# Performance work log

Hardware: AMD Instinct MI355X
Metric: run time of the kernel (lower is better)

Reference implementation:

```python
import jax, jax.numpy as jnp
import numpy as np

DIM = 1024
INTER = 1024
N_EXPERTS = 16
TOPK = 4
SHARED_INTER = 2 * INTER  # n_shared_experts * moe_inter_dim
T = 8192


def setup_inputs() -> dict:
    key = jax.random.key(0)
    ks = jax.random.split(key, 15)
    s = 0.02
    inp = {
        "x": jax.random.normal(ks[0], (T, DIM), jnp.float32),
        "gate_w": jax.random.normal(ks[1], (N_EXPERTS, DIM), jnp.float32) * s,
        # routed experts, stacked over expert axis
        "ew1": jax.random.normal(ks[2], (N_EXPERTS, INTER, DIM), jnp.float32) * s,
        "eb1": jax.random.normal(ks[3], (N_EXPERTS, INTER), jnp.float32) * s,
        "ew2": jax.random.normal(ks[4], (N_EXPERTS, DIM, INTER), jnp.float32) * s,
        "eb2": jax.random.normal(ks[5], (N_EXPERTS, DIM), jnp.float32) * s,
        "ew3": jax.random.normal(ks[6], (N_EXPERTS, INTER, DIM), jnp.float32) * s,
        "eb3": jax.random.normal(ks[7], (N_EXPERTS, INTER), jnp.float32) * s,
        # shared expert MLP (inter = 2 * moe_inter_dim)
        "sw1": jax.random.normal(ks[8], (SHARED_INTER, DIM), jnp.float32) * s,
        "sb1": jax.random.normal(ks[9], (SHARED_INTER,), jnp.float32) * s,
        "sw2": jax.random.normal(ks[10], (DIM, SHARED_INTER), jnp.float32) * s,
        "sb2": jax.random.normal(ks[11], (DIM,), jnp.float32) * s,
        "sw3": jax.random.normal(ks[12], (SHARED_INTER, DIM), jnp.float32) * s,
        "sb3": jax.random.normal(ks[13], (SHARED_INTER,), jnp.float32) * s,
    }
    return inp


def _ffn(x, w1, b1, w2, b2, w3, b3):
    # w2(silu(w1(x)) * w3(x))
    return (jax.nn.silu(x @ w1.T + b1) * (x @ w3.T + b3)) @ w2.T + b2


def reference(x, gate_w, ew1, eb1, ew2, eb2, ew3, eb3, sw1, sb1, sw2, sb2, sw3, sb3):
    # Gate: softmax scores in fp32 (n_groups=1 -> no group masking), top-k routing
    scores = jax.nn.softmax((x @ gate_w.T).astype(jnp.float32), axis=-1)  # [T, E]
    top_vals, idx = jax.lax.top_k(scores, TOPK)  # [T, K]
    weights = top_vals.astype(x.dtype)  # route_scale = 1.0, softmax score_func

    # Per-expert combine weight: zero for unselected experts.
    nT = x.shape[0]
    cw = jnp.zeros((nT, N_EXPERTS), x.dtype).at[
        jnp.arange(nT)[:, None], idx
    ].add(weights)  # [T, E]

    # Routed experts: masked-dense dispatch (weight 0 kills unselected terms)
    y = jnp.zeros_like(x)
    for e in range(N_EXPERTS):
        y = y + cw[:, e:e + 1] * _ffn(x, ew1[e], eb1[e], ew2[e], eb2[e], ew3[e], eb3[e])

    # Shared experts (always applied)
    z = _ffn(x, sw1, sb1, sw2, sb2, sw3, sb3)
    return y + z
```

## Files before the change

### kernel.cpp

```cpp
#include <hip/hip_runtime.h>
#include <cstdint>
#include <cstddef>

#define TOK     8192
#define DIMD    1024
#define INTERD  1024
#define NEXP    16
#define SINTER  2048
#define CAP256  36864
#define MAXT    144
#define HBLK    32

typedef __bf16 bf16_t;
typedef __bf16 bf16x8_t __attribute__((ext_vector_type(8)));
typedef __bf16 bf16x4_t __attribute__((ext_vector_type(4)));
typedef float  f32x4_t  __attribute__((ext_vector_type(4)));

__device__ __forceinline__ void gload_lds16(const bf16_t* g, bf16_t* l) {
  __builtin_amdgcn_global_load_lds((const __attribute__((address_space(1))) void*)g,
                                   (__attribute__((address_space(3))) void*)l,
                                   16, 0, 0);
}

__global__ void init_kernel(int* toklist, float* wtlist, int* tile_e, int* tile_rs) {
  int i = blockIdx.x * blockDim.x + threadIdx.x;
  if (i < CAP256) { toklist[i] = -1; wtlist[i] = 0.0f; }
  if (i < 512)    { tile_e[i] = -1; tile_rs[i] = 0; }
}

__global__ void cvt_kernel(const float* __restrict__ in, bf16_t* __restrict__ out, int n4) {
  int stride = gridDim.x * blockDim.x;
  for (int i = blockIdx.x * blockDim.x + threadIdx.x; i < n4; i += stride) {
    float4 v = ((const float4*)in)[i];
    bf16x4_t o;
    o[0] = (bf16_t)v.x; o[1] = (bf16_t)v.y; o[2] = (bf16_t)v.z; o[3] = (bf16_t)v.w;
    ((bf16x4_t*)out)[i] = o;
  }
}

__global__ void cvt_ileave(const float* __restrict__ s1, const float* __restrict__ s3,
                           bf16_t* __restrict__ dst, int total4, int esh) {
  int stride = gridDim.x * blockDim.x;
  int fmask = (1 << esh) - 1;
  for (int i = blockIdx.x * blockDim.x + threadIdx.x; i < total4; i += stride) {
    int k4 = i & 255;
    int fr = i >> 8;
    int e  = fr >> esh;
    int f  = fr & fmask;
    int p  = f >> 4, s = f & 15;
    int real = ((p >> 1) << 4) + s;
    size_t srow = ((size_t)e << (esh - 1)) + real;
    const float* src = ((p & 1) ? s3 : s1) + (srow << 10) + (k4 << 2);
    float4 v = *(const float4*)src;
    bf16x4_t o;
    o[0] = (bf16_t)v.x; o[1] = (bf16_t)v.y; o[2] = (bf16_t)v.z; o[3] = (bf16_t)v.w;
    ((bf16x4_t*)dst)[i] = o;
  }
}

__global__ __launch_bounds__(256)
void gate_kernel(const float* __restrict__ x, const float* __restrict__ gw,
                 int* __restrict__ tkidx, float* __restrict__ tkwt) {
  int wv = threadIdx.x >> 6, lane = threadIdx.x & 63;
  int t = blockIdx.x * 4 + wv;
  const float4* xp = (const float4*)(x + (size_t)t * DIMD + lane * 16);
  float4 xv[4];
#pragma unroll
  for (int i = 0; i < 4; ++i) xv[i] = xp[i];
  float sc[NEXP];
#pragma unroll
  for (int e = 0; e < NEXP; ++e) {
    const float4* wp = (const float4*)(gw + (size_t)e * DIMD + lane * 16);
    float s = 0.0f;
#pragma unroll
    for (int i = 0; i < 4; ++i) {
      float4 w = wp[i];
      s += xv[i].x * w.x + xv[i].y * w.y + xv[i].z * w.z + xv[i].w * w.w;
    }
    sc[e] = s;
  }
#pragma unroll
  for (int off = 32; off > 0; off >>= 1)
#pragma unroll
    for (int e = 0; e < NEXP; ++e)
      sc[e] += __shfl_xor(sc[e], off, 64);
  if (lane == 0) {
    float m = sc[0];
#pragma unroll
    for (int e = 1; e < NEXP; ++e) m = fmaxf(m, sc[e]);
    float p[NEXP], s = 0.0f;
#pragma unroll
    for (int e = 0; e < NEXP; ++e) { p[e] = __expf(sc[e] - m); s += p[e]; }
    float inv = 1.0f / s;
    unsigned used = 0;
    for (int k = 0; k < 4; ++k) {
      int best = 0; float bv = -1.0f;
#pragma unroll
      for (int e = 0; e < NEXP; ++e)
        if (!((used >> e) & 1u) && p[e] > bv) { bv = p[e]; best = e; }
      used |= 1u << best;
      tkidx[t * 4 + k] = best;
      tkwt[t * 4 + k] = bv * inv;
    }
  }
}

__global__ __launch_bounds__(256)
void hist_kernel(const int* __restrict__ tkidx, int* __restrict__ blkhist) {
  __shared__ int h[NEXP];
  if (threadIdx.x < NEXP) h[threadIdx.x] = 0;
  __syncthreads();
  int4 v = ((const int4*)tkidx)[blockIdx.x * 256 + threadIdx.x];
  atomicAdd(&h[v.x], 1);
  atomicAdd(&h[v.y], 1);
  atomicAdd(&h[v.z], 1);
  atomicAdd(&h[v.w], 1);
  __syncthreads();
  if (threadIdx.x < NEXP) blkhist[blockIdx.x * NEXP + threadIdx.x] = h[threadIdx.x];
}

__global__ void offs_kernel(const int* __restrict__ blkhist, int* __restrict__ offsets,
                            int* __restrict__ blkbase,
                            int* __restrict__ tile_e, int* __restrict__ tile_rs) {
  if (threadIdx.x != 0 || blockIdx.x != 0) return;
  int counts[NEXP];
  for (int e = 0; e < NEXP; ++e) {
    int s = 0;
    for (int b = 0; b < HBLK; ++b) s += blkhist[b * NEXP + e];
    counts[e] = s;
  }
  int off = 0, nt = 0;
  for (int e = 0; e < NEXP; ++e) {
    offsets[e] = off;
    int c = counts[e];
    int ntile = (c + 255) >> 8;
    for (int i = 0; i < ntile; ++i) { tile_e[nt] = e; tile_rs[nt] = off + (i << 8); ++nt; }
    off += ntile << 8;
  }
  offsets[NEXP] = off;
  for (int e = 0; e < NEXP; ++e) {
    int base = offsets[e];
    for (int b = 0; b < HBLK; ++b) {
      blkbase[b * NEXP + e] = base;
      base += blkhist[b * NEXP + e];
    }
  }
}

__global__ __launch_bounds__(256)
void scat_kernel(const int* __restrict__ tkidx, const float* __restrict__ tkwt,
                 const int* __restrict__ blkbase,
                 int* __restrict__ toklist, float* __restrict__ wtlist) {
  __shared__ int cur[NEXP];
  if (threadIdx.x < NEXP) cur[threadIdx.x] = blkbase[blockIdx.x * NEXP + threadIdx.x];
  __syncthreads();
  int idx = blockIdx.x * 256 + threadIdx.x;
  int4 v = ((const int4*)tkidx)[idx];
  float4 w = ((const float4*)tkwt)[idx];
  int p0 = atomicAdd(&cur[v.x], 1); toklist[p0] = idx; wtlist[p0] = w.x;
  int p1 = atomicAdd(&cur[v.y], 1); toklist[p1] = idx; wtlist[p1] = w.y;
  int p2 = atomicAdd(&cur[v.z], 1); toklist[p2] = idx; wtlist[p2] = w.z;
  int p3 = atomicAdd(&cur[v.w], 1); toklist[p3] = idx; wtlist[p3] = w.w;
}

#define SBAR __builtin_amdgcn_sched_barrier(0)

template <bool TABLE, int EPI>
__global__ __launch_bounds__(512, 2)
void gemm8p(const bf16_t* __restrict__ Ag, const bf16_t* __restrict__ Bw,
            const float* __restrict__ bias1, const float* __restrict__ bias3,
            void* __restrict__ Outp,
            const int* __restrict__ tile_e, const int* __restrict__ tile_rs,
            const int* __restrict__ toklist, const float* __restrict__ wtlist,
            int K, int ldOut, size_t strideB, int biasStride) {
  constexpr int BM = 256, BN = 256;
  __shared__ __align__(16) bf16_t lds[65536];

  int rowstart, e = 0;
  if constexpr (TABLE) {
    e = tile_e[blockIdx.y];
    if (e < 0) return;
    rowstart = tile_rs[blockIdx.y];
  } else {
    rowstart = blockIdx.y * BM;
  }
  const bf16_t* Bwp = Bw + (TABLE ? (size_t)e * strideB : (size_t)0);
  const int boff = TABLE ? e * biasStride : 0;

  const int tid = threadIdx.x, lane = tid & 63, wv = tid >> 6;
  const int wm = wv >> 2, wn = wv & 3;
  const int xsw = (lane & 7) << 4;
  const int klo = (lane >> 4) * 16;

  const bf16_t* srcp[8];
#pragma unroll
  for (int h = 0; h < 2; ++h)
#pragma unroll
    for (int j = 0; j < 2; ++j) {
      int idx = tid + j * 512;
      int r = h * 128 + (idx >> 3);
      int slot = (idx & 7) ^ ((idx >> 3) & 7);
      long arow;
      if constexpr (TABLE && EPI == 0) {
        int t = toklist[rowstart + r];
        arow = (t < 0) ? 0 : t;
      } else {
        arow = rowstart + r;
      }
      srcp[h * 2 + j] = Ag + (size_t)arow * K + slot * 8;
      int br = (int)blockIdx.x * BN + r;
      srcp[4 + h * 2 + j] = Bwp + (size_t)br * K + slot * 8;
    }

#define STG_HT(HB, H, NB, KT)                                                   \
  do {                                                                          \
    bf16_t* d_ = (bf16_t*)lds + (NB) * 32768 + (HB) * 16384 + (H) * 8192 + tid * 8; \
    gload_lds16(srcp[(HB) * 4 + (H) * 2 + 0] + (KT) * 64, d_);                  \
    gload_lds16(srcp[(HB) * 4 + (H) * 2 + 1] + (KT) * 64, d_ + 4096);           \
  } while (0)

  f32x4_t acc[8][4] = {};
  bf16x8_t bfr[4];

#define PHASE(KS, MH, STG, WT, BUFB, NB, KT1)                                   \
  do {                                                                          \
    bf16x8_t afr[4];                                                            \
    _Pragma("unroll")                                                           \
    for (int q = 0; q < 4; ++q) {                                               \
      int rl = wm * 64 + q * 16 + (lane & 15);                                  \
      afr[q] = *(const bf16x8_t*)((BUFB) + (MH) * 16384 +                       \
                 ((rl * 128 + (KS) * 64 + klo) ^ xsw));                         \
    }                                                                           \
    if ((MH) == 0) {                                                            \
      _Pragma("unroll")                                                         \
      for (int ni = 0; ni < 4; ++ni) {                                          \
        int ct = wn * 64 + ni * 16 + (lane & 15);                               \
        bfr[ni] = *(const bf16x8_t*)((BUFB) + 32768 + (ct >> 7) * 16384 +       \
                   (((ct & 127) * 128 + (KS) * 64 + klo) ^ xsw));               \
      }                                                                         \
    }                                                                           \
    if ((STG) == 1) {                                                           \
      STG_HT(0, 0, NB, KT1);                                                    \
      STG_HT(1, 0, NB, KT1);                                                    \
      STG_HT(1, 1, NB, KT1);                                                    \
    } else if ((STG) == 2) {                                                    \
      STG_HT(0, 1, NB, KT1);                                                    \
    }                                                                           \
    SBAR;                                                                       \
    if ((WT) == 1) asm volatile("s_waitcnt vmcnt(6)" ::: "memory");             \
    else if ((WT) == 2) asm volatile("s_waitcnt vmcnt(2)" ::: "memory");        \
    else if ((WT) == 3) asm volatile("s_waitcnt vmcnt(0)" ::: "memory");        \
    SBAR;                                                                       \
    __builtin_amdgcn_s_barrier();                                               \
    asm volatile("s_waitcnt lgkmcnt(0)" ::: "memory");                          \
    SBAR;                                                                       \
    __builtin_amdgcn_s_setprio(1);                                              \
    _Pragma("unroll")                                                           \
    for (int q = 0; q < 4; ++q)                                                 \
      _Pragma("unroll")                                                         \
      for (int ni = 0; ni < 4; ++ni)                                            \
        acc[(MH) * 4 + q][ni] = __builtin_amdgcn_mfma_f32_16x16x32_bf16(        \
            afr[q], bfr[ni], acc[(MH) * 4 + q][ni], 0, 0, 0);                   \
    __builtin_amdgcn_s_setprio(0);                                              \
    __builtin_amdgcn_s_barrier();                                               \
    SBAR;                                                                       \
  } while (0)

  const int NTK = K >> 6;

  STG_HT(0, 0, 0, 0);
  STG_HT(1, 0, 0, 0);
  STG_HT(1, 1, 0, 0);
  STG_HT(0, 1, 0, 0);
  SBAR;
  asm volatile("s_waitcnt vmcnt(0)" ::: "memory");
  SBAR;
  __builtin_amdgcn_s_barrier();
  SBAR;

  for (int kt = 0; kt < NTK - 1; ++kt) {
    const char* bufb = (const char*)lds + (kt & 1) * 65536;
    int nb = (kt + 1) & 1, k1 = kt + 1;
    PHASE(0, 0, 1, 1, bufb, nb, k1);
    PHASE(0, 1, 2, 0, bufb, nb, k1);
    PHASE(1, 0, 0, 0, bufb, nb, k1);
    PHASE(1, 1, 0, 2, bufb, nb, k1);
  }
  {
    const char* bufb = (const char*)lds + ((NTK - 1) & 1) * 65536;
    PHASE(0, 0, 0, 3, bufb, 0, 0);
    PHASE(0, 1, 0, 0, bufb, 0, 0);
    PHASE(1, 0, 0, 0, bufb, 0, 0);
    PHASE(1, 1, 0, 0, bufb, 0, 0);
  }

  if constexpr (EPI == 0) {
    float b1v[2], b3v[2];
    int rcbase = (int)blockIdx.x * 128 + wn * 32 + (lane & 15);
#pragma unroll
    for (int ni2 = 0; ni2 < 2; ++ni2) {
      b1v[ni2] = bias1[boff + rcbase + ni2 * 16];
      b3v[ni2] = bias3[boff + rcbase + ni2 * 16];
    }
    bf16_t* Hout = (bf16_t*)Outp;
#pragma unroll
    for (int mi = 0; mi < 8; ++mi)
#pragma unroll
      for (int rg = 0; rg < 4; ++rg) {
        int Rb = (mi < 4) ? (wm * 64 + mi * 16) : (128 + wm * 64 + (mi - 4) * 16);
        int rt = Rb + ((lane >> 4) << 2) + rg;
        int grow = rowstart + rt;
        float wt = 1.0f;
        if constexpr (TABLE) wt = wtlist[grow];
        size_t ob = (size_t)grow * ldOut + rcbase;
#pragma unroll
        for (int ni2 = 0; ni2 < 2; ++ni2) {
          float v1 = acc[mi][2 * ni2][rg] + b1v[ni2];
          float v3 = acc[mi][2 * ni2 + 1][rg] + b3v[ni2];
          float sg = v1 / (1.0f + __expf(-v1));
          Hout[ob + ni2 * 16] = (bf16_t)(sg * v3 * wt);
        }
      }
  } else {
    float bv[4];
    int colbase = (int)blockIdx.x * BN + wn * 64 + (lane & 15);
#pragma unroll
    for (int ni = 0; ni < 4; ++ni) bv[ni] = bias1[boff + colbase + ni * 16];
    float* Fout = (float*)Outp;
#pragma unroll
    for (int mi = 0; mi < 8; ++mi)
#pragma unroll
      for (int rg = 0; rg < 4; ++rg) {
        int Rb = (mi < 4) ? (wm * 64 + mi * 16) : (128 + wm * 64 + (mi - 4) * 16);
        int rt = Rb + ((lane >> 4) << 2) + rg;
        int grow = rowstart + rt;
        if constexpr (EPI == 1) {
          int t = toklist[grow];
          float wt = wtlist[grow];
          if (t >= 0) {
            size_t ob = (size_t)t * ldOut + colbase;
#pragma unroll
            for (int ni = 0; ni < 4; ++ni)
              atomicAdd(&Fout[ob + ni * 16], acc[mi][ni][rg] + wt * bv[ni]);
          }
        } else {
          size_t ob = (size_t)grow * ldOut + colbase;
#pragma unroll
          for (int ni = 0; ni < 4; ++ni)
            Fout[ob + ni * 16] = acc[mi][ni][rg] + bv[ni];
        }
      }
  }
#undef PHASE
#undef STG_HT
}

extern "C" void kernel_launch(void* const* d_in, const int* in_sizes, int n_in,
                              void* d_out, int out_size, void* d_ws, size_t ws_size,
                              hipStream_t stream) {
  const float* x   = (const float*)d_in[0];
  const float* gw  = (const float*)d_in[1];
  const float* ew1 = (const float*)d_in[2];
  const float* eb1 = (const float*)d_in[3];
  const float* ew2 = (const float*)d_in[4];
  const float* eb2 = (const float*)d_in[5];
  const float* ew3 = (const float*)d_in[6];
  const float* eb3 = (const float*)d_in[7];
  const float* sw1 = (const float*)d_in[8];
  const float* sb1 = (const float*)d_in[9];
  const float* sw2 = (const float*)d_in[10];
  const float* sb2 = (const float*)d_in[11];
  const float* sw3 = (const float*)d_in[12];
  const float* sb3 = (const float*)d_in[13];
  float* out = (float*)d_out;
  (void)ws_size;

  char* ws = (char*)d_ws;
  size_t off = 0;
  auto alloc = [&](size_t bytes) -> void* {
    off = (off + 255) & ~(size_t)255;
    void* p = ws + off;
    off += bytes;
    return p;
  };

  bf16_t* xb    = (bf16_t*)alloc((size_t)TOK * DIMD * 2);
  bf16_t* ew13i = (bf16_t*)alloc((size_t)NEXP * 2 * INTERD * DIMD * 2);
  bf16_t* ew2b  = (bf16_t*)alloc((size_t)NEXP * DIMD * INTERD * 2);
  bf16_t* sw13i = (bf16_t*)alloc((size_t)2 * SINTER * DIMD * 2);
  bf16_t* sw2b  = (bf16_t*)alloc((size_t)DIMD * SINTER * 2);
  bf16_t* Hun   = (bf16_t*)alloc((size_t)CAP256 * INTERD * 2);
  bf16_t* Hs    = Hun;
  bf16_t* Hg    = Hun;
  int*   toklist = (int*)alloc(CAP256 * 4);
  float* wtlist  = (float*)alloc(CAP256 * 4);
  int*   offsets = (int*)alloc((NEXP + 1) * 4);
  int*   blkhist = (int*)alloc(HBLK * NEXP * 4);
  int*   blkbase = (int*)alloc(HBLK * NEXP * 4);
  int*   tile_e  = (int*)alloc(512 * 4);
  int*   tile_rs = (int*)alloc(512 * 4);
  int*   tkidx   = (int*)alloc((size_t)TOK * 4 * 4);
  float* tkwt    = (float*)alloc((size_t)TOK * 4 * 4);

  init_kernel<<<(CAP256 + 255) / 256, 256, 0, stream>>>(toklist, wtlist, tile_e, tile_rs);

  cvt_kernel<<<2048, 256, 0, stream>>>(x,   xb,   TOK * DIMD / 4);
  cvt_kernel<<<2048, 256, 0, stream>>>(ew2, ew2b, NEXP * DIMD * INTERD / 4);
  cvt_kernel<<<512,  256, 0, stream>>>(sw2, sw2b, DIMD * SINTER / 4);
  cvt_ileave<<<2048, 256, 0, stream>>>(ew1, ew3, ew13i, NEXP * 2 * INTERD * DIMD / 4, 11);
  cvt_ileave<<<1024, 256, 0, stream>>>(sw1, sw3, sw13i, 2 * SINTER * DIMD / 4, 12);

  gate_kernel<<<TOK / 4, 256, 0, stream>>>(x, gw, tkidx, tkwt);
  hist_kernel<<<HBLK, 256, 0, stream>>>(tkidx, blkhist);
  offs_kernel<<<1, 64, 0, stream>>>(blkhist, offsets, blkbase, tile_e, tile_rs);
  scat_kernel<<<HBLK, 256, 0, stream>>>(tkidx, tkwt, blkbase, toklist, wtlist);

  gemm8p<false, 0><<<dim3(2 * SINTER / 256, TOK / 256), 512, 0, stream>>>(
      xb, sw13i, sb1, sb3, Hs, nullptr, nullptr, nullptr, nullptr,
      DIMD, SINTER, 0, 0);
  gemm8p<false, 2><<<dim3(DIMD / 256, TOK / 256), 512, 0, stream>>>(
      Hs, sw2b, sb2, nullptr, out, nullptr, nullptr, nullptr, nullptr,
      SINTER, DIMD, 0, 0);

  gemm8p<true, 0><<<dim3(2 * INTERD / 256, MAXT), 512, 0, stream>>>(
      xb, ew13i, eb1, eb3, Hg, tile_e, tile_rs, toklist, wtlist,
      DIMD, INTERD, (size_t)2 * INTERD * DIMD, INTERD);
  gemm8p<true, 1><<<dim3(DIMD / 256, MAXT), 512, 0, stream>>>(
      Hg, ew2b, eb2, nullptr, out, tile_e, tile_rs, toklist, wtlist,
      INTERD, DIMD, (size_t)DIMD * INTERD, DIMD);
}
```

Baseline: 626.6 us.

## Rework GEMM to 4-stage K=32 pipeline and replace atomic scatter with gather-fuse

Replaces the double-buffered K=64 GEMM with a 4-deep ring of K=32 stages using unswizzled k-slab LDS layout, and makes the row tile size a template parameter, using BM=128 for the shared down-projection. The routed down-projection now writes per-slot bf16 outputs instead of doing fp32 atomicAdd into the output. A new fuse kernel gathers the four expert slots per token via positions recorded in the scatter kernel. This aims to remove atomic contention and improve latency hiding, but adds an extra pass over memory, rounds expert outputs to bf16, and drops the XOR swizzle, which may cause LDS bank conflicts.

```diff
diff --git a/kernel.cpp b/kernel.cpp
--- a/kernel.cpp
+++ b/kernel.cpp
@@ -21,6 +21,16 @@
                                    (__attribute__((address_space(3))) void*)l,
                                    16, 0, 0);
 }
+
+template <int N> __device__ __forceinline__ void vmwait() {
+  if constexpr (N == 0)      asm volatile("s_waitcnt vmcnt(0)" ::: "memory");
+  else if constexpr (N == 3) asm volatile("s_waitcnt vmcnt(3)" ::: "memory");
+  else if constexpr (N == 4) asm volatile("s_waitcnt vmcnt(4)" ::: "memory");
+  else if constexpr (N == 6) asm volatile("s_waitcnt vmcnt(6)" ::: "memory");
+  else if constexpr (N == 8) asm volatile("s_waitcnt vmcnt(8)" ::: "memory");
+}
+
+#define SBAR __builtin_amdgcn_sched_barrier(0)
 
 __global__ void init_kernel(int* toklist, float* wtlist, int* tile_e, int* tile_rs) {
   int i = blockIdx.x * blockDim.x + threadIdx.x;
@@ -150,7 +160,8 @@
 __global__ __launch_bounds__(256)
 void scat_kernel(const int* __restrict__ tkidx, const float* __restrict__ tkwt,
                  const int* __restrict__ blkbase,
-                 int* __restrict__ toklist, float* __restrict__ wtlist) {
+                 int* __restrict__ toklist, float* __restrict__ wtlist,
+                 int4* __restrict__ pos4) {
   __shared__ int cur[NEXP];
   if (threadIdx.x < NEXP) cur[threadIdx.x] = blkbase[blockIdx.x * NEXP + threadIdx.x];
   __syncthreads();
@@ -161,20 +172,44 @@
   int p1 = atomicAdd(&cur[v.y], 1); toklist[p1] = idx; wtlist[p1] = w.y;
   int p2 = atomicAdd(&cur[v.z], 1); toklist[p2] = idx; wtlist[p2] = w.z;
   int p3 = atomicAdd(&cur[v.w], 1); toklist[p3] = idx; wtlist[p3] = w.w;
-}
-
-#define SBAR __builtin_amdgcn_sched_barrier(0)
-
-template <bool TABLE, int EPI>
+  pos4[idx] = make_int4(p0, p1, p2, p3);
+}
+
+__global__ __launch_bounds__(256)
+void fuse_kernel(const int4* __restrict__ pos4, const bf16_t* __restrict__ Yg,
+                 float* __restrict__ out) {
+  int t = blockIdx.x;
+  int4 p = pos4[t];
+  int c = threadIdx.x;
+  float4 o = ((const float4*)(out + (size_t)t * DIMD))[c];
+  bf16x4_t y0 = ((const bf16x4_t*)(Yg + (size_t)p.x * DIMD))[c];
+  bf16x4_t y1 = ((const bf16x4_t*)(Yg + (size_t)p.y * DIMD))[c];
+  bf16x4_t y2 = ((const bf16x4_t*)(Yg + (size_t)p.z * DIMD))[c];
+  bf16x4_t y3 = ((const bf16x4_t*)(Yg + (size_t)p.w * DIMD))[c];
+  o.x += (float)y0[0] + (float)y1[0] + (float)y2[0] + (float)y3[0];
+  o.y += (float)y0[1] + (float)y1[1] + (float)y2[1] + (float)y3[1];
+  o.z += (float)y0[2] + (float)y1[2] + (float)y2[2] + (float)y3[2];
+  o.w += (float)y0[3] + (float)y1[3] + (float)y2[3] + (float)y3[3];
+  ((float4*)(out + (size_t)t * DIMD))[c] = o;
+}
+
+template <int BM, bool TABLE, int EPI>
 __global__ __launch_bounds__(512, 2)
-void gemm8p(const bf16_t* __restrict__ Ag, const bf16_t* __restrict__ Bw,
+void gemm4b(const bf16_t* __restrict__ Ag, const bf16_t* __restrict__ Bw,
             const float* __restrict__ bias1, const float* __restrict__ bias3,
             void* __restrict__ Outp,
             const int* __restrict__ tile_e, const int* __restrict__ tile_rs,
             const int* __restrict__ toklist, const float* __restrict__ wtlist,
             int K, int ldOut, size_t strideB, int biasStride) {
-  constexpr int BM = 256, BN = 256;
-  __shared__ __align__(16) bf16_t lds[65536];
+  constexpr int BN = 256;
+  constexpr int MI = BM / 32;
+  constexpr int NG = MI / 4;
+  constexpr int RB = (BM == 256) ? 8 : 7;
+  constexpr int AJ = BM / 128;
+  constexpr int ABY = BM * 64;
+  constexpr int BUFBY = ABY + 16384;
+  constexpr int LPT = AJ + 2;
+  __shared__ __align__(16) bf16_t lds[4 * BUFBY / 2];
 
   int rowstart, e = 0;
   if constexpr (TABLE) {
@@ -189,110 +224,77 @@
 
   const int tid = threadIdx.x, lane = tid & 63, wv = tid >> 6;
   const int wm = wv >> 2, wn = wv & 3;
-  const int xsw = (lane & 7) << 4;
-  const int klo = (lane >> 4) * 16;
-
-  const bf16_t* srcp[8];
-#pragma unroll
-  for (int h = 0; h < 2; ++h)
-#pragma unroll
-    for (int j = 0; j < 2; ++j) {
-      int idx = tid + j * 512;
-      int r = h * 128 + (idx >> 3);
-      int slot = (idx & 7) ^ ((idx >> 3) & 7);
-      long arow;
-      if constexpr (TABLE && EPI == 0) {
-        int t = toklist[rowstart + r];
-        arow = (t < 0) ? 0 : t;
-      } else {
-        arow = rowstart + r;
-      }
-      srcp[h * 2 + j] = Ag + (size_t)arow * K + slot * 8;
-      int br = (int)blockIdx.x * BN + r;
-      srcp[4 + h * 2 + j] = Bwp + (size_t)br * K + slot * 8;
-    }
-
-#define STG_HT(HB, H, NB, KT)                                                   \
+
+  int rA = tid & ((1 << RB) - 1);
+  int ksA = tid >> RB;
+  long arow;
+  if constexpr (TABLE && EPI == 0) {
+    int t = toklist[rowstart + rA];
+    arow = (t < 0) ? 0 : t;
+  } else {
+    arow = rowstart + rA;
+  }
+  const bf16_t* srcA = Ag + (size_t)arow * K + ksA * 8;
+  int rBr = tid & 255, ksB = tid >> 8;
+  const bf16_t* srcB = Bwp + (size_t)((int)blockIdx.x * BN + rBr) * K + ksB * 8;
+
+#define STAGE(KT)                                                               \
   do {                                                                          \
-    bf16_t* d_ = (bf16_t*)lds + (NB) * 32768 + (HB) * 16384 + (H) * 8192 + tid * 8; \
-    gload_lds16(srcp[(HB) * 4 + (H) * 2 + 0] + (KT) * 64, d_);                  \
-    gload_lds16(srcp[(HB) * 4 + (H) * 2 + 1] + (KT) * 64, d_ + 4096);           \
+    bf16_t* db_ = (bf16_t*)lds + ((KT) & 3) * (BUFBY / 2);                      \
+    _Pragma("unroll")                                                           \
+    for (int j_ = 0; j_ < AJ; ++j_)                                             \
+      gload_lds16(srcA + (KT) * 32 + j_ * ((512 >> RB) * 8),                    \
+                  db_ + j_ * 4096 + tid * 8);                                   \
+    _Pragma("unroll")                                                           \
+    for (int j_ = 0; j_ < 2; ++j_)                                              \
+      gload_lds16(srcB + (KT) * 32 + j_ * 16,                                   \
+                  db_ + ABY / 2 + j_ * 4096 + tid * 8);                         \
   } while (0)
 
-  f32x4_t acc[8][4] = {};
-  bf16x8_t bfr[4];
-
-#define PHASE(KS, MH, STG, WT, BUFB, NB, KT1)                                   \
+  f32x4_t acc[MI][4] = {};
+
+#define TILE(VMN, DOSTG)                                                        \
   do {                                                                          \
-    bf16x8_t afr[4];                                                            \
+    vmwait<VMN>(); SBAR;                                                        \
+    __builtin_amdgcn_s_barrier(); SBAR;                                         \
+    if (DOSTG) STAGE(kt + 3);                                                   \
+    const char* bufb = (const char*)lds + (kt & 3) * BUFBY;                     \
+    bf16x8_t bfr[4];                                                            \
     _Pragma("unroll")                                                           \
-    for (int q = 0; q < 4; ++q) {                                               \
-      int rl = wm * 64 + q * 16 + (lane & 15);                                  \
-      afr[q] = *(const bf16x8_t*)((BUFB) + (MH) * 16384 +                       \
-                 ((rl * 128 + (KS) * 64 + klo) ^ xsw));                         \
+    for (int ni = 0; ni < 4; ++ni) {                                            \
+      int ct = wn * 64 + ni * 16 + (lane & 15);                                 \
+      bfr[ni] = *(const bf16x8_t*)(bufb + ABY + (lane >> 4) * 4096 + ct * 16);  \
     }                                                                           \
-    if ((MH) == 0) {                                                            \
+    _Pragma("unroll")                                                           \
+    for (int g = 0; g < NG; ++g) {                                              \
+      bf16x8_t afr[4];                                                          \
       _Pragma("unroll")                                                         \
-      for (int ni = 0; ni < 4; ++ni) {                                          \
-        int ct = wn * 64 + ni * 16 + (lane & 15);                               \
-        bfr[ni] = *(const bf16x8_t*)((BUFB) + 32768 + (ct >> 7) * 16384 +       \
-                   (((ct & 127) * 128 + (KS) * 64 + klo) ^ xsw));               \
+      for (int q = 0; q < 4; ++q) {                                             \
+        int row = wm * (BM / 2) + (g * 4 + q) * 16 + (lane & 15);               \
+        afr[q] = *(const bf16x8_t*)(bufb + (lane >> 4) * (BM * 16) + row * 16); \
       }                                                                         \
+      asm volatile("s_waitcnt lgkmcnt(0)" ::: "memory"); SBAR;                  \
+      __builtin_amdgcn_s_setprio(1);                                            \
+      _Pragma("unroll")                                                         \
+      for (int q = 0; q < 4; ++q)                                               \
+        _Pragma("unroll")                                                       \
+        for (int ni = 0; ni < 4; ++ni)                                          \
+          acc[g * 4 + q][ni] = __builtin_amdgcn_mfma_f32_16x16x32_bf16(         \
+              afr[q], bfr[ni], acc[g * 4 + q][ni], 0, 0, 0);                    \
+      __builtin_amdgcn_s_setprio(0); SBAR;                                      \
     }                                                                           \
-    if ((STG) == 1) {                                                           \
-      STG_HT(0, 0, NB, KT1);                                                    \
-      STG_HT(1, 0, NB, KT1);                                                    \
-      STG_HT(1, 1, NB, KT1);                                                    \
-    } else if ((STG) == 2) {                                                    \
-      STG_HT(0, 1, NB, KT1);                                                    \
-    }                                                                           \
-    SBAR;                                                                       \
-    if ((WT) == 1) asm volatile("s_waitcnt vmcnt(6)" ::: "memory");             \
-    else if ((WT) == 2) asm volatile("s_waitcnt vmcnt(2)" ::: "memory");        \
-    else if ((WT) == 3) asm volatile("s_waitcnt vmcnt(0)" ::: "memory");        \
-    SBAR;                                                                       \
-    __builtin_amdgcn_s_barrier();                                               \
-    asm volatile("s_waitcnt lgkmcnt(0)" ::: "memory");                          \
-    SBAR;                                                                       \
-    __builtin_amdgcn_s_setprio(1);                                              \
-    _Pragma("unroll")                                                           \
-    for (int q = 0; q < 4; ++q)                                                 \
-      _Pragma("unroll")                                                         \
-      for (int ni = 0; ni < 4; ++ni)                                            \
-        acc[(MH) * 4 + q][ni] = __builtin_amdgcn_mfma_f32_16x16x32_bf16(        \
-            afr[q], bfr[ni], acc[(MH) * 4 + q][ni], 0, 0, 0);                   \
-    __builtin_amdgcn_s_setprio(0);                                              \
-    __builtin_amdgcn_s_barrier();                                               \
-    SBAR;                                                                       \
   } while (0)
 
-  const int NTK = K >> 6;
-
-  STG_HT(0, 0, 0, 0);
-  STG_HT(1, 0, 0, 0);
-  STG_HT(1, 1, 0, 0);
-  STG_HT(0, 1, 0, 0);
-  SBAR;
-  asm volatile("s_waitcnt vmcnt(0)" ::: "memory");
-  SBAR;
-  __builtin_amdgcn_s_barrier();
-  SBAR;
-
-  for (int kt = 0; kt < NTK - 1; ++kt) {
-    const char* bufb = (const char*)lds + (kt & 1) * 65536;
-    int nb = (kt + 1) & 1, k1 = kt + 1;
-    PHASE(0, 0, 1, 1, bufb, nb, k1);
-    PHASE(0, 1, 2, 0, bufb, nb, k1);
-    PHASE(1, 0, 0, 0, bufb, nb, k1);
-    PHASE(1, 1, 0, 2, bufb, nb, k1);
-  }
-  {
-    const char* bufb = (const char*)lds + ((NTK - 1) & 1) * 65536;
-    PHASE(0, 0, 0, 3, bufb, 0, 0);
-    PHASE(0, 1, 0, 0, bufb, 0, 0);
-    PHASE(1, 0, 0, 0, bufb, 0, 0);
-    PHASE(1, 1, 0, 0, bufb, 0, 0);
-  }
+  const int NTK = K >> 5;
+
+  STAGE(0); STAGE(1); STAGE(2);
+
+  int kt = 0;
+  for (; kt < NTK - 2; ++kt) {
+    TILE(2 * LPT, kt + 3 < NTK);
+  }
+  TILE(LPT, false); ++kt;
+  TILE(0, false);
 
   if constexpr (EPI == 0) {
     float b1v[2], b3v[2];
@@ -304,11 +306,10 @@
     }
     bf16_t* Hout = (bf16_t*)Outp;
 #pragma unroll
-    for (int mi = 0; mi < 8; ++mi)
+    for (int mi = 0; mi < MI; ++mi)
 #pragma unroll
       for (int rg = 0; rg < 4; ++rg) {
-        int Rb = (mi < 4) ? (wm * 64 + mi * 16) : (128 + wm * 64 + (mi - 4) * 16);
-        int rt = Rb + ((lane >> 4) << 2) + rg;
+        int rt = wm * (BM / 2) + mi * 16 + ((lane >> 4) << 2) + rg;
         int grow = rowstart + rt;
         float wt = 1.0f;
         if constexpr (TABLE) wt = wtlist[grow];
@@ -321,6 +322,24 @@
           Hout[ob + ni2 * 16] = (bf16_t)(sg * v3 * wt);
         }
       }
+  } else if constexpr (EPI == 1) {
+    float bv[4];
+    int colbase = (int)blockIdx.x * BN + wn * 64 + (lane & 15);
+#pragma unroll
+    for (int ni = 0; ni < 4; ++ni) bv[ni] = bias1[boff + colbase + ni * 16];
+    bf16_t* Yout = (bf16_t*)Outp;
+#pragma unroll
+    for (int mi = 0; mi < MI; ++mi)
+#pragma unroll
+      for (int rg = 0; rg < 4; ++rg) {
+        int rt = wm * (BM / 2) + mi * 16 + ((lane >> 4) << 2) + rg;
+        int grow = rowstart + rt;
+        float wt = wtlist[grow];
+        size_t ob = (size_t)grow * ldOut + colbase;
+#pragma unroll
+        for (int ni = 0; ni < 4; ++ni)
+          Yout[ob + ni * 16] = (bf16_t)(acc[mi][ni][rg] + wt * bv[ni]);
+      }
   } else {
     float bv[4];
     int colbase = (int)blockIdx.x * BN + wn * 64 + (lane & 15);
@@ -328,31 +347,19 @@
     for (int ni = 0; ni < 4; ++ni) bv[ni] = bias1[boff + colbase + ni * 16];
     float* Fout = (float*)Outp;
 #pragma unroll
-    for (int mi = 0; mi < 8; ++mi)
+    for (int mi = 0; mi < MI; ++mi)
 #pragma unroll
       for (int rg = 0; rg < 4; ++rg) {
-        int Rb = (mi < 4) ? (wm * 64 + mi * 16) : (128 + wm * 64 + (mi - 4) * 16);
-        int rt = Rb + ((lane >> 4) << 2) + rg;
+        int rt = wm * (BM / 2) + mi * 16 + ((lane >> 4) << 2) + rg;
         int grow = rowstart + rt;
-        if constexpr (EPI == 1) {
-          int t = toklist[grow];
-          float wt = wtlist[grow];
-          if (t >= 0) {
-            size_t ob = (size_t)t * ldOut + colbase;
-#pragma unroll
-            for (int ni = 0; ni < 4; ++ni)
-              atomicAdd(&Fout[ob + ni * 16], acc[mi][ni][rg] + wt * bv[ni]);
-          }
-        } else {
-          size_t ob = (size_t)grow * ldOut + colbase;
-#pragma unroll
-          for (int ni = 0; ni < 4; ++ni)
-            Fout[ob + ni * 16] = acc[mi][ni][rg] + bv[ni];
-        }
+        size_t ob = (size_t)grow * ldOut + colbase;
+#pragma unroll
+        for (int ni = 0; ni < 4; ++ni)
+          Fout[ob + ni * 16] = acc[mi][ni][rg] + bv[ni];
       }
   }
-#undef PHASE
-#undef STG_HT
+#undef TILE
+#undef STAGE
 }
 
 extern "C" void kernel_launch(void* const* d_in, const int* in_sizes, int n_in,
@@ -392,6 +399,7 @@
   bf16_t* Hun   = (bf16_t*)alloc((size_t)CAP256 * INTERD * 2);
   bf16_t* Hs    = Hun;
   bf16_t* Hg    = Hun;
+  bf16_t* Yg    = xb;
   int*   toklist = (int*)alloc(CAP256 * 4);
   float* wtlist  = (float*)alloc(CAP256 * 4);
   int*   offsets = (int*)alloc((NEXP + 1) * 4);
@@ -401,6 +409,7 @@
   int*   tile_rs = (int*)alloc(512 * 4);
   int*   tkidx   = (int*)alloc((size_t)TOK * 4 * 4);
   float* tkwt    = (float*)alloc((size_t)TOK * 4 * 4);
+  int4*  pos4    = (int4*)alloc((size_t)TOK * 16);
 
   init_kernel<<<(CAP256 + 255) / 256, 256, 0, stream>>>(toklist, wtlist, tile_e, tile_rs);
 
@@ -413,19 +422,21 @@
   gate_kernel<<<TOK / 4, 256, 0, stream>>>(x, gw, tkidx, tkwt);
   hist_kernel<<<HBLK, 256, 0, stream>>>(tkidx, blkhist);
   offs_kernel<<<1, 64, 0, stream>>>(blkhist, offsets, blkbase, tile_e, tile_rs);
-  scat_kernel<<<HBLK, 256, 0, stream>>>(tkidx, tkwt, blkbase, toklist, wtlist);
-
-  gemm8p<false, 0><<<dim3(2 * SINTER / 256, TOK / 256), 512, 0, stream>>>(
+  scat_kernel<<<HBLK, 256, 0, stream>>>(tkidx, tkwt, blkbase, toklist, wtlist, pos4);
+
+  gemm4b<256, false, 0><<<dim3(2 * SINTER / 256, TOK / 256), 512, 0, stream>>>(
       xb, sw13i, sb1, sb3, Hs, nullptr, nullptr, nullptr, nullptr,
       DIMD, SINTER, 0, 0);
-  gemm8p<false, 2><<<dim3(DIMD / 256, TOK / 256), 512, 0, stream>>>(
+  gemm4b<128, false, 2><<<dim3(DIMD / 256, TOK / 128), 512, 0, stream>>>(
       Hs, sw2b, sb2, nullptr, out, nullptr, nullptr, nullptr, nullptr,
       SINTER, DIMD, 0, 0);
 
-  gemm8p<true, 0><<<dim3(2 * INTERD / 256, MAXT), 512, 0, stream>>>(
+  gemm4b<256, true, 0><<<dim3(2 * INTERD / 256, MAXT), 512, 0, stream>>>(
       xb, ew13i, eb1, eb3, Hg, tile_e, tile_rs, toklist, wtlist,
       DIMD, INTERD, (size_t)2 * INTERD * DIMD, INTERD);
-  gemm8p<true, 1><<<dim3(DIMD / 256, MAXT), 512, 0, stream>>>(
-      Hg, ew2b, eb2, nullptr, out, tile_e, tile_rs, toklist, wtlist,
+  gemm4b<256, true, 1><<<dim3(DIMD / 256, MAXT), 512, 0, stream>>>(
+      Hg, ew2b, eb2, nullptr, Yg, tile_e, tile_rs, toklist, wtlist,
       INTERD, DIMD, (size_t)DIMD * INTERD, DIMD);
-}
+
+  fuse_kernel<<<TOK, 256, 0, stream>>>(pos4, Yg, out);
+}
```

Result: slower. 731.2 us (+16.7%).
